# Performance work log

Hardware: AMD Instinct MI355X
Metric: run time of the kernel (lower is better)

## Reference

```python
import jax, jax.numpy as jnp
import numpy as np

B, ENC_T, DEC_T = 16, 512, 800
D = 256    # pos_att_dim == att_dim == encoder dim
H = 1024   # attention rnn dim
M = 8      # num gmm mixtures
DELTA_MIN_LIMIT = 0.0
DELTA_OFFSET = 0.0


def setup_inputs() -> dict:
    key = jax.random.key(0)
    ks = jax.random.split(key, 12)
    s = 0.05  # small init so sigmoids/tanh stay in sane range
    b_lin = jnp.concatenate([jnp.zeros((M,)), jnp.zeros((M,)), 3.0 * jnp.ones((M,))])
    return {
        'encoder_outputs': jax.random.normal(ks[0], (B, ENC_T, D), jnp.float32),
        'melenc_outputs': jax.random.normal(ks[1], (B, DEC_T, D), jnp.float32),
        'encoder_lengths': jax.random.randint(ks[2], (B,), ENC_T // 2, ENC_T + 1),
        'output_lengths': jax.random.randint(ks[3], (B,), DEC_T // 2, DEC_T + 1),
        'cond_lens': jax.random.randint(ks[4], (B,), ENC_T // 2, ENC_T + 1),
        'W_ih': jax.random.normal(ks[5], (4 * H, 3 * D), jnp.float32) * s,
        'W_hh': jax.random.normal(ks[6], (4 * H, H), jnp.float32) * s,
        'b_ih': jnp.zeros((4 * H,), jnp.float32),
        'b_hh': jnp.zeros((4 * H,), jnp.float32),
        'W1': jax.random.normal(ks[7], (D, H), jnp.float32) * s,
        'b1': jnp.zeros((D,), jnp.float32),
        'W2': jax.random.normal(ks[8], (D, D), jnp.float32) * s,
        'W_lin': jax.random.normal(ks[9], (3 * M, D), jnp.float32) * 0.01,  # lin.weight.data.mul_(0.01)
        'b_lin': b_lin,
    }


def reference(encoder_outputs, melenc_outputs, encoder_lengths, output_lengths,
              cond_lens, W_ih, W_hh, b_ih, b_hh, W1, b1, W2, W_lin, b_lin):
    Bb, enc_T, Dd = encoder_outputs.shape
    dec_T = melenc_outputs.shape[1]
    n_mix = W_lin.shape[0] // 3
    Hh = W_hh.shape[1]
    dtype = encoder_outputs.dtype

    pos = jnp.arange(enc_T, dtype=dtype)                      # [enc_T]
    cond_f = cond_lens.astype(dtype)
    enc_mask = (pos[None, :] < cond_f[:, None]).astype(dtype)  # [B, enc_T]
    cond_min1 = cond_f - 1.0                                   # [B]
    # dec-step validity mask (get_mask_3d decoder axis), [dec_T, B]
    dec_valid = (jnp.arange(dec_T)[:, None] < output_lengths[None, :]).astype(dtype)

    def lstm_cell(x, h, c):
        g = x @ W_ih.T + b_ih + h @ W_hh.T + b_hh   # [B, 4H]
        i, f, gg, o = jnp.split(g, 4, axis=-1)
        c2 = jax.nn.sigmoid(f) * c + jax.nn.sigmoid(i) * jnp.tanh(gg)
        h2 = jax.nn.sigmoid(o) * jnp.tanh(c2)
        return h2, c2

    def step(carry, xs):
        h, c, ctx, nctx, loc = carry
        mel, vdec = xs                              # mel [B,D], vdec [B]
        q = jnp.concatenate([mel, ctx, nctx], axis=-1)  # [B, 3D]
        h, c = lstm_cell(q, h, c)
        # F network: Linear -> LeakyReLU(0.1) -> Linear(no bias) -> Tanh -> lin
        x = h @ W1.T + b1
        x = jnp.where(x >= 0, x, 0.1 * x)
        x = jnp.tanh(x @ W2.T)
        out = x @ W_lin.T + b_lin                   # [B, 3M]
        w_, d_, s_ = jnp.split(out, 3, axis=-1)
        w = jax.nn.softmax(w_, axis=-1)             # [B, M]
        std = jax.nn.sigmoid(s_)
        delta = jax.nn.sigmoid(d_) + 0.005
        if DELTA_MIN_LIMIT > 0.0:
            delta = jnp.maximum(delta, DELTA_MIN_LIMIT)
        if DELTA_OFFSET > 0.0:
            delta = delta + DELTA_OFFSET
        loc = loc + delta                           # [B, M]
        # tanh-CDF difference over positions: [B, enc_T, M]
        diff = loc[:, None, :] - pos[None, :, None]
        upper = jnp.tanh((diff + 0.5) / std[:, None, :])   # uses pos - 0.5
        lower = jnp.tanh((diff - 0.5) / std[:, None, :])   # uses pos + 0.5
        z = (upper - lower) * 0.5
        align = jnp.einsum('bem,bm->be', z, w)      # [B, enc_T]
        align = align * enc_mask * vdec[:, None]    # masked_fill_(mask, 0.0)
        next_w = jnp.roll(align, 1, axis=-1)
        ctx = jnp.einsum('be,bed->bd', align, encoder_outputs)
        nctx = jnp.einsum('be,bed->bd', next_w, encoder_outputs)
        # loc = loc - (loc - (cond_lens-1)).clamp(min=0)
        loc = loc - jnp.maximum(loc - cond_min1[:, None], 0.0)
        return (h, c, ctx, nctx, loc), (ctx, align)

    init = (jnp.zeros((Bb, Hh), dtype), jnp.zeros((Bb, Hh), dtype),
            jnp.zeros((Bb, Dd), dtype), encoder_outputs[:, 0, :],
            jnp.full((Bb, n_mix), -0.1, dtype))
    xs = (jnp.swapaxes(melenc_outputs, 0, 1), dec_valid)
    _, (ctxs, aligns) = jax.lax.scan(step, init, xs)
    attention_context = jnp.swapaxes(ctxs, 0, 1)    # [B, dec_T, D]
    attention_weights = jnp.swapaxes(aligns, 0, 1)  # [B, dec_T, enc_T]
    # final mask on attention_context over decoder steps
    attention_context = attention_context * jnp.swapaxes(dec_valid, 0, 1)[:, :, None]
    return attention_context, attention_weights
```

## Files before the change

kernel.cpp:

```cpp
#include <hip/hip_runtime.h>
#include <stdint.h>

#define DEV static __device__ __forceinline__

namespace {
constexpr int Bx = 16, ENCx = 512, DECx = 800, Dx = 256, Hx = 1024;
constexpr int NBLK = 256, NTHR = 512;
constexpr int NCHAIN = 32;

constexpr int WS_H    = 0;
constexpr int WS_X1M  = WS_H + 2*Bx*Hx;
constexpr int WS_CTX  = WS_X1M + 2*Bx*Dx;
constexpr int WS_FEND = WS_CTX + 2*2*Bx*Dx;
constexpr int IW_HC  = 0;
constexpr int IW_XC  = IW_HC + 801*16;
constexpr int IW_CC  = IW_XC + 800*16;
constexpr int IW_END = IW_CC + 800*16;
constexpr size_t CTXOUT = (size_t)Bx*DECx*Dx;

constexpr int LH_STR = 1028;
constexpr int CT_STR = 260;
constexpr int LW_H   = 0;
constexpr int LW_WHH = LW_H + 16*LH_STR;
constexpr int LDS_DYN_F = LW_WHH + 16384;
constexpr size_t SMEM_BYTES = (size_t)LDS_DYN_F * 4;
}

DEV float frcp(float x){ return __builtin_amdgcn_rcpf(x); }
DEV float sigm(float x){ return frcp(1.0f + __expf(-x)); }
DEV float ftanh(float x){
  x = fminf(fmaxf(x, -15.0f), 15.0f);
  float e = __expf(2.0f*x);
  return (e - 1.0f) * frcp(e + 1.0f);
}
DEV float wred16(float v){
  v += __shfl_xor(v, 1); v += __shfl_xor(v, 2);
  v += __shfl_xor(v, 4); v += __shfl_xor(v, 8);
  return v;
}
DEV int   ld_rlx(const int* p){ return __hip_atomic_load(p, __ATOMIC_RELAXED, __HIP_MEMORY_SCOPE_AGENT); }
DEV float ldf_c(const float* p){ return __hip_atomic_load(p, __ATOMIC_RELAXED, __HIP_MEMORY_SCOPE_AGENT); }
DEV void  stf_c(float* p, float v){ __hip_atomic_store(p, v, __ATOMIC_RELAXED, __HIP_MEMORY_SCOPE_AGENT); }
DEV void  add_cnt(int* p){ __hip_atomic_fetch_add(p, 1, __ATOMIC_RELAXED, __HIP_MEMORY_SCOPE_AGENT); }
DEV void cbar(){ asm volatile("" ::: "memory"); }

DEV void spin_fma(){
  float x = 1.0f;
  #pragma unroll
  for (int i = 0; i < 16; ++i) x = fmaf(x, 1.0000001f, 1e-9f);
  asm volatile("" :: "v"(x));
}

DEV void ld8_wait(float4 (&r)[8], const float* p){
  const float *a1=p+2048,*a2=p+4096,*a3=p+6144,*a4=p+8192,*a5=p+10240,*a6=p+12288,*a7=p+14336;
  asm volatile(
    "global_load_dwordx4 %0, %8, off sc1\n\t"
    "global_load_dwordx4 %1, %9, off sc1\n\t"
    "global_load_dwordx4 %2, %10, off sc1\n\t"
    "global_load_dwordx4 %3, %11, off sc1\n\t"
    "global_load_dwordx4 %4, %12, off sc1\n\t"
    "global_load_dwordx4 %5, %13, off sc1\n\t"
    "global_load_dwordx4 %6, %14, off sc1\n\t"
    "global_load_dwordx4 %7, %15, off sc1\n\t"
    "s_waitcnt vmcnt(0)"
    : "=&v"(r[0]),"=&v"(r[1]),"=&v"(r[2]),"=&v"(r[3]),
      "=&v"(r[4]),"=&v"(r[5]),"=&v"(r[6]),"=&v"(r[7])
    : "v"(p),"v"(a1),"v"(a2),"v"(a3),"v"(a4),"v"(a5),"v"(a6),"v"(a7)
    : "memory");
}
DEV void ld4_wait(float4 (&r)[4], const float* p){
  const float *a1=p+2048,*a2=p+4096,*a3=p+6144;
  asm volatile(
    "global_load_dwordx4 %0, %4, off sc1\n\t"
    "global_load_dwordx4 %1, %5, off sc1\n\t"
    "global_load_dwordx4 %2, %6, off sc1\n\t"
    "global_load_dwordx4 %3, %7, off sc1\n\t"
    "s_waitcnt vmcnt(0)"
    : "=&v"(r[0]),"=&v"(r[1]),"=&v"(r[2]),"=&v"(r[3])
    : "v"(p),"v"(a1),"v"(a2),"v"(a3)
    : "memory");
}

DEV void wait_cnt(int* p, int target, volatile int* lslot, int stamp){
  const int tid = threadIdx.x;
  if (tid < 64){
    while (ld_rlx(p) < target) spin_fma();
    if (tid == 0) *lslot = stamp;
  } else {
    while (*lslot < stamp) spin_fma();
  }
  __syncthreads();
  cbar();
}

DEV void gchunk(float (&acc)[2][4], float4 wa, float4 wb, const float* xlane, size_t xstride, int b4){
  #pragma unroll
  for (int bi = 0; bi < 4; ++bi){
    float4 xv = *reinterpret_cast<const float4*>(xlane + (size_t)(b4*4 + bi)*xstride);
    acc[0][bi] = fmaf(wa.x,xv.x, fmaf(wa.y,xv.y, fmaf(wa.z,xv.z, fmaf(wa.w,xv.w, acc[0][bi]))));
    acc[1][bi] = fmaf(wb.x,xv.x, fmaf(wb.y,xv.y, fmaf(wb.z,xv.z, fmaf(wb.w,xv.w, acc[1][bi]))));
  }
}

extern "C" __global__ void gmm_init(float* wsf){
  int* wsi = (int*)(wsf + WS_FEND);
  int idx = blockIdx.x*blockDim.x + threadIdx.x;
  for (int k = idx; k < IW_END; k += gridDim.x*blockDim.x) wsi[k] = 0;
}

extern "C" __global__ void __launch_bounds__(NTHR, 1) gmm_main(
    const float* __restrict__ enc, const float* __restrict__ mel,
    const int* __restrict__ outlen, const int* __restrict__ condlen,
    const float* __restrict__ Wih, const float* __restrict__ Whh,
    const float* __restrict__ bih, const float* __restrict__ bhh,
    const float* __restrict__ W1,  const float* __restrict__ b1v,
    const float* __restrict__ W2,  const float* __restrict__ Wlin,
    const float* __restrict__ blin,
    float* __restrict__ out, float* __restrict__ wsf)
{
  const int bk = blockIdx.x, tid = threadIdx.x;
  const int lane = tid & 63;
  const int klane4 = (tid & 15) * 4;
  const int b4 = (tid >> 4) & 3;
  const int wid = tid >> 6;

  int* wsi  = (int*)(wsf + WS_FEND);
  int* hCnt = wsi + IW_HC;
  int* xCnt = wsi + IW_XC;
  int* cCnt = wsi + IW_CC;
  float* hm   = wsf + WS_H;
  float* x1m  = wsf + WS_X1M;
  float* ctxm = wsf + WS_CTX;

  extern __shared__ float lds[];
  float* lh   = lds + LW_H;
  float* lwhh = lds + LW_WHH;

  __shared__ float g_lds[256];
  __shared__ float bsum[16];
  __shared__ float cl[64];
  __shared__ float x1l[256];
  __shared__ float x2p[512];
  __shared__ float x2l[256];
  __shared__ float outp[384];
  __shared__ float outl[24];
  __shared__ float mixw[8], mixlc[8], mixis[8];
  __shared__ float locl[8];
  __shared__ float albl[512];
  __shared__ float cpn[2][4][128];
  __shared__ int   s_cond, s_olen;
  __shared__ int   lfh, lfx, lfc;

  if (tid == 0){ lfh = 0; lfx = 0; lfc = 0; }

  const int jidx0 = 2*wid;
  const int j0 = (jidx0 >> 2)*1024 + bk*4 + (jidx0 & 3);
  const int j1 = ((jidx0+1) >> 2)*1024 + bk*4 + ((jidx0+1) & 3);
  const float* WihR0 = Wih + (size_t)j0*768;
  const float* WihR1 = Wih + (size_t)j1*768;

  const bool is_chain = (bk < NCHAIN);
  const int  cb  = bk >> 1;
  const int  hf2 = bk & 1;

  #pragma unroll
  for (int jj = jidx0; jj <= jidx0 + 1; ++jj){
    const int gj = (jj >> 2)*1024 + bk*4 + (jj & 3);
    float4* dst = (float4*)(lwhh + jj*1024);
    const float4* s = (const float4*)(Whh + (size_t)gj*1024);
    for (int i = lane; i < 256; i += 64) dst[i] = s[i];
  }
  if (tid < 16){
    int g = tid >> 2, ul = tid & 3, u = bk*4 + ul;
    bsum[tid] = bih[g*1024 + u] + bhh[g*1024 + u];
  }
  float4 w2r[32];
  if (is_chain){
    if (tid == 0){ s_cond = condlen[cb]; s_olen = outlen[cb]; }
    if (tid < 8) locl[tid] = -0.1f;
    int r = tid >> 1, hf = tid & 1;
    const float* w2row = W2 + (size_t)r*256 + hf*128;
    #pragma unroll
    for (int i = 0; i < 32; ++i) w2r[i] = *reinterpret_cast<const float4*>(w2row + i*4);
  }
  __syncthreads();

  auto write_h = [&](int t){
    float4 r[8];
    ld8_wait(r, hm + (t & 1)*(Bx*Hx) + tid*4);
    #pragma unroll
    for (int i = 0; i < 8; ++i){
      int rr = 2*i + (tid >> 8);
      *reinterpret_cast<float4*>(lh + rr*LH_STR + (tid & 255)*4) = r[i];
    }
    __syncthreads();
  };

  {
    float acc[2][4] = {{0,0,0,0},{0,0,0,0}};
    #pragma unroll
    for (int it = 0; it < 4; ++it){
      int k = it*64 + klane4;
      gchunk(acc, *(const float4*)(WihR0 + k), *(const float4*)(WihR1 + k),
             mel + k, (size_t)DECx*Dx, b4);
    }
    #pragma unroll
    for (int it = 0; it < 4; ++it){
      int k = it*64 + klane4;
      gchunk(acc, *(const float4*)(WihR0 + 512 + k), *(const float4*)(WihR1 + 512 + k),
             enc + k, (size_t)ENCx*Dx, b4);
    }
    #pragma unroll
    for (int jj = 0; jj < 2; ++jj)
      #pragma unroll
      for (int bi = 0; bi < 4; ++bi){
        float v = wred16(acc[jj][bi]);
        if ((tid & 15) == 0) g_lds[(jidx0 + jj)*16 + b4*4 + bi] = v;
      }
    __syncthreads();
    if (tid < 64){
      int b = tid & 15, ul = tid >> 4, u = bk*4 + ul;
      float gi = g_lds[( 0 + ul)*16 + b] + bsum[ul];
      float gg = g_lds[( 8 + ul)*16 + b] + bsum[8 + ul];
      float go = g_lds[(12 + ul)*16 + b] + bsum[12 + ul];
      float c2 = sigm(gi) * ftanh(gg);
      float h2 = sigm(go) * ftanh(c2);
      cl[b*4 + ul] = c2;
      stf_c(hm + b*1024 + u, h2);
    }
    __syncthreads();
    if (tid == 0) add_cnt(hCnt + 0*16);
  }

  for (int t = 0; t < DECx; ++t){
    const int par = t & 1;
    const bool last = (t == DECx - 1);

    wait_cnt(hCnt + t*16, NBLK, &lfh, t + 1);
    write_h(t);
    if (tid < 256){
      int b = tid >> 4, kl = tid & 15;
      const float* W1r = W1 + (size_t)bk*1024;
      float a = 0.f;
      #pragma unroll
      for (int it = 0; it < 16; ++it){
        int k = it*64 + kl*4;
        float4 wv = *reinterpret_cast<const float4*>(W1r + k);
        float4 xv = *reinterpret_cast<const float4*>(lh + (size_t)b*LH_STR + k);
        a = fmaf(wv.x,xv.x, fmaf(wv.y,xv.y, fmaf(wv.z,xv.z, fmaf(wv.w,xv.w, a))));
      }
      a = wred16(a);
      if (kl == 0){
        a += b1v[bk];
        a = (a >= 0.f) ? a : 0.1f*a;
        stf_c(x1m + par*(Bx*Dx) + b*256 + bk, a);
      }
    }
    __syncthreads();
    if (tid == 0) add_cnt(xCnt + t*16);

    float acc[2][4] = {{0,0,0,0},{0,0,0,0}};

    if (is_chain){
      wait_cnt(xCnt + t*16, NBLK, &lfx, t + 1);
      if (tid < 256) x1l[tid] = ldf_c(x1m + par*(Bx*Dx) + cb*256 + tid);
      __syncthreads();
      {
        int hf = tid & 1;
        const float* x1b = x1l + hf*128;
        float a = 0.f;
        #pragma unroll
        for (int i = 0; i < 32; ++i){
          float4 xv = *(const float4*)(x1b + i*4);
          a = fmaf(w2r[i].x,xv.x, fmaf(w2r[i].y,xv.y, fmaf(w2r[i].z,xv.z, fmaf(w2r[i].w,xv.w, a))));
        }
        x2p[tid] = a;
      }
      __syncthreads();
      if (tid < 256) x2l[tid] = ftanh(x2p[2*tid] + x2p[2*tid + 1]);
      __syncthreads();
      if (tid < 384){
        int r = tid >> 4, ks = tid & 15;
        const float* wr = Wlin + (size_t)r*256 + ks*16;
        const float* xb = x2l + ks*16;
        float s = 0.f;
        #pragma unroll
        for (int k = 0; k < 16; ++k) s = fmaf(xb[k], wr[k], s);
        outp[tid] = s;
      }
      __syncthreads();
      if (tid < 24){
        float s = blin[tid];
        #pragma unroll
        for (int j = 0; j < 16; ++j) s += outp[tid*16 + j];
        outl[tid] = s;
      }
      __syncthreads();
      if (tid < 8){
        float w = outl[tid];
        float mx = w;
        mx = fmaxf(mx, __shfl_xor(mx, 1)); mx = fmaxf(mx, __shfl_xor(mx, 2)); mx = fmaxf(mx, __shfl_xor(mx, 4));
        float e = __expf(w - mx);
        float sum = e;
        sum += __shfl_xor(sum, 1); sum += __shfl_xor(sum, 2); sum += __shfl_xor(sum, 4);
        mixw[tid] = e * frcp(sum);
        float cm1 = (float)s_cond - 1.0f;
        float dl = sigm(outl[8 + tid]) + 0.005f;
        float lc = locl[tid] + dl;
        mixlc[tid] = lc;
        locl[tid]  = fminf(lc, cm1);
        mixis[tid] = 1.0f + __expf(-outl[16 + tid]);
      }
      __syncthreads();
      {
        int e = tid;
        float ef = (float)e;
        float a = 0.f;
        #pragma unroll
        for (int m = 0; m < 8; ++m){
          float df = mixlc[m] - ef;
          a += (ftanh((df + 0.5f)*mixis[m]) - ftanh((df - 0.5f)*mixis[m])) * mixw[m];
        }
        a *= 0.5f;
        bool valid = (e < s_cond) && (t < s_olen);
        if (!valid) a = 0.f;
        albl[e] = a;
        if (hf2 == 0)
          out[CTXOUT + (size_t)cb*((size_t)DECx*ENCx) + (size_t)t*ENCx + e] = a;
      }
      __syncthreads();
      {
        int dl = tid & 127, eg = tid >> 7;
        const float* encb = enc + (size_t)cb*ENCx*Dx + hf2*128;
        float ca = 0.f, na = 0.f;
        #pragma unroll 4
        for (int i = 0; i < 128; ++i){
          int e = eg*128 + i;
          float av = albl[e];
          float nv = albl[(e + 511) & 511];
          float ev = encb[(size_t)e*256 + dl];
          ca = fmaf(av, ev, ca);
          na = fmaf(nv, ev, na);
        }
        cpn[0][eg][dl & 127] = 0.f;
        cpn[0][eg][dl] = ca;
        cpn[1][eg][dl] = na;
      }
      __syncthreads();
      if (tid < 256){
        int z = tid >> 7, dd = tid & 127;
        float s = cpn[z][0][dd] + cpn[z][1][dd] + cpn[z][2][dd] + cpn[z][3][dd];
        int d = hf2*128 + dd;
        stf_c(ctxm + par*(2*Bx*Dx) + z*(Bx*Dx) + cb*256 + d, s);
        if (z == 0)
          out[(size_t)cb*((size_t)DECx*Dx) + (size_t)t*Dx + d] = s;
      }
      __syncthreads();
      if (tid == 0) add_cnt(cCnt + t*16);
      if (!last){
        const float* melt = mel + (size_t)(t + 1)*Dx;
        #pragma unroll
        for (int it = 0; it < 4; ++it){
          int k = it*64 + klane4;
          gchunk(acc, *(const float4*)(WihR0 + k), *(const float4*)(WihR1 + k),
                 melt + k, (size_t)DECx*Dx, b4);
        }
        #pragma unroll 4
        for (int it = 0; it < 16; ++it){
          int k = it*64 + klane4;
          gchunk(acc, *(const float4*)(lwhh + jidx0*1024 + k), *(const float4*)(lwhh + (jidx0+1)*1024 + k),
                 lh + k, LH_STR, b4);
        }
      }
    } else {
      if (!last){
        const float* melt = mel + (size_t)(t + 1)*Dx;
        #pragma unroll
        for (int it = 0; it < 4; ++it){
          int k = it*64 + klane4;
          gchunk(acc, *(const float4*)(WihR0 + k), *(const float4*)(WihR1 + k),
                 melt + k, (size_t)DECx*Dx, b4);
        }
        #pragma unroll 4
        for (int it = 0; it < 16; ++it){
          int k = it*64 + klane4;
          gchunk(acc, *(const float4*)(lwhh + jidx0*1024 + k), *(const float4*)(lwhh + (jidx0+1)*1024 + k),
                 lh + k, LH_STR, b4);
        }
      }
    }

    if (!last){
      wait_cnt(cCnt + t*16, NCHAIN, &lfc, t + 1);
      {
        float4 cr[4];
        ld4_wait(cr, ctxm + par*(2*Bx*Dx) + tid*4);
        #pragma unroll
        for (int i = 0; i < 4; ++i){
          int r = 8*i + (tid >> 6);
          *reinterpret_cast<float4*>(lh + r*CT_STR + (tid & 63)*4) = cr[i];
        }
      }
      __syncthreads();
      #pragma unroll
      for (int it = 0; it < 4; ++it){
        int k = it*64 + klane4;
        gchunk(acc, *(const float4*)(WihR0 + 256 + k), *(const float4*)(WihR1 + 256 + k),
               lh + k, CT_STR, b4);
      }
      #pragma unroll
      for (int it = 0; it < 4; ++it){
        int k = it*64 + klane4;
        gchunk(acc, *(const float4*)(WihR0 + 512 + k), *(const float4*)(WihR1 + 512 + k),
               lh + 16*CT_STR + k, CT_STR, b4);
      }
      #pragma unroll
      for (int jj = 0; jj < 2; ++jj)
        #pragma unroll
        for (int bi = 0; bi < 4; ++bi){
          float v = wred16(acc[jj][bi]);
          if ((tid & 15) == 0) g_lds[(jidx0 + jj)*16 + b4*4 + bi] = v;
        }
      __syncthreads();
      if (tid < 64){
        int b = tid & 15, ul = tid >> 4, u = bk*4 + ul;
        float gi = g_lds[( 0 + ul)*16 + b] + bsum[ul];
        float gf = g_lds[( 4 + ul)*16 + b] + bsum[4 + ul];
        float gg = g_lds[( 8 + ul)*16 + b] + bsum[8 + ul];
        float go = g_lds[(12 + ul)*16 + b] + bsum[12 + ul];
        float co = cl[b*4 + ul];
        float c2 = sigm(gf)*co + sigm(gi)*ftanh(gg);
        float h2 = sigm(go)*ftanh(c2);
        cl[b*4 + ul] = c2;
        stf_c(hm + ((t + 1) & 1)*(Bx*Hx) + b*1024 + u, h2);
      }
      __syncthreads();
      if (tid == 0) add_cnt(hCnt + (t + 1)*16);
    }
  }
}

extern "C" void kernel_launch(void* const* d_in, const int* in_sizes, int n_in,
                              void* d_out, int out_size, void* d_ws, size_t ws_size,
                              hipStream_t stream)
{
  const float* enc    = (const float*)d_in[0];
  const float* mel    = (const float*)d_in[1];
  const int*   outlen = (const int*)d_in[3];
  const int*   cond   = (const int*)d_in[4];
  const float* Wih    = (const float*)d_in[5];
  const float* Whh    = (const float*)d_in[6];
  const float* bih    = (const float*)d_in[7];
  const float* bhh    = (const float*)d_in[8];
  const float* W1     = (const float*)d_in[9];
  const float* b1v    = (const float*)d_in[10];
  const float* W2     = (const float*)d_in[11];
  const float* Wlin   = (const float*)d_in[12];
  const float* blin   = (const float*)d_in[13];
  float* outp = (float*)d_out;
  float* wsf  = (float*)d_ws;

  (void)hipFuncSetAttribute((const void*)gmm_main,
                            hipFuncAttributeMaxDynamicSharedMemorySize,
                            (int)SMEM_BYTES);

  hipLaunchKernelGGL(gmm_init, dim3(64), dim3(256), 0, stream, wsf);

  void* args[] = {
    (void*)&enc, (void*)&mel, (void*)&outlen, (void*)&cond,
    (void*)&Wih, (void*)&Whh, (void*)&bih, (void*)&bhh,
    (void*)&W1, (void*)&b1v, (void*)&W2, (void*)&Wlin, (void*)&blin,
    (void*)&outp, (void*)&wsf
  };
  (void)hipLaunchCooperativeKernel((void*)gmm_main, dim3(NBLK), dim3(NTHR),
                                   args, SMEM_BYTES, stream);
}
```

Measured before the change: 60.04 ms.

## Split persistent kernel into gate and chain blocks with bf16 exchange and slot flags

```diff
diff --git a/kernel.cpp b/kernel.cpp
--- a/kernel.cpp
+++ b/kernel.cpp
@@ -5,17 +5,19 @@
 
 namespace {
 constexpr int Bx = 16, ENCx = 512, DECx = 800, Dx = 256, Hx = 1024;
-constexpr int NBLK = 256, NTHR = 512;
-constexpr int NCHAIN = 32;
-
-constexpr int WS_H    = 0;
-constexpr int WS_X1M  = WS_H + 2*Bx*Hx;
-constexpr int WS_CTX  = WS_X1M + 2*Bx*Dx;
-constexpr int WS_FEND = WS_CTX + 2*2*Bx*Dx;
-constexpr int IW_HC  = 0;
-constexpr int IW_XC  = IW_HC + 801*16;
-constexpr int IW_CC  = IW_XC + 800*16;
-constexpr int IW_END = IW_CC + 800*16;
+constexpr int NGATE = 128, NCHAIN = 32, NBLK = NGATE + NCHAIN, NTHR = 512;
+
+constexpr int WS_HBH  = 0;
+constexpr int WS_CTXH = WS_HBH + 16384;
+constexpr int WS_X1M  = WS_CTXH + 8192;
+constexpr int WS_FEND = WS_X1M + 8192;
+constexpr int IW_HSLOT = 0;
+constexpr int IW_XSLOT = 128;
+constexpr int IW_CSLOT = 256;
+constexpr int IW_HRDY  = 320;
+constexpr int IW_XRDY  = 448;
+constexpr int IW_CRDY  = 576;
+constexpr int IW_END   = 704;
 constexpr size_t CTXOUT = (size_t)Bx*DECx*Dx;
 
 constexpr int LH_STR = 1028;
@@ -39,35 +41,22 @@
   return v;
 }
 DEV int   ld_rlx(const int* p){ return __hip_atomic_load(p, __ATOMIC_RELAXED, __HIP_MEMORY_SCOPE_AGENT); }
+DEV void  st_rlx(int* p, int v){ __hip_atomic_store(p, v, __ATOMIC_RELAXED, __HIP_MEMORY_SCOPE_AGENT); }
+DEV void  st_rlx_u32(unsigned* p, unsigned v){ __hip_atomic_store(p, v, __ATOMIC_RELAXED, __HIP_MEMORY_SCOPE_AGENT); }
 DEV float ldf_c(const float* p){ return __hip_atomic_load(p, __ATOMIC_RELAXED, __HIP_MEMORY_SCOPE_AGENT); }
 DEV void  stf_c(float* p, float v){ __hip_atomic_store(p, v, __ATOMIC_RELAXED, __HIP_MEMORY_SCOPE_AGENT); }
-DEV void  add_cnt(int* p){ __hip_atomic_fetch_add(p, 1, __ATOMIC_RELAXED, __HIP_MEMORY_SCOPE_AGENT); }
 DEV void cbar(){ asm volatile("" ::: "memory"); }
 
-DEV void spin_fma(){
-  float x = 1.0f;
-  #pragma unroll
-  for (int i = 0; i < 16; ++i) x = fmaf(x, 1.0000001f, 1e-9f);
-  asm volatile("" :: "v"(x));
-}
-
-DEV void ld8_wait(float4 (&r)[8], const float* p){
-  const float *a1=p+2048,*a2=p+4096,*a3=p+6144,*a4=p+8192,*a5=p+10240,*a6=p+12288,*a7=p+14336;
-  asm volatile(
-    "global_load_dwordx4 %0, %8, off sc1\n\t"
-    "global_load_dwordx4 %1, %9, off sc1\n\t"
-    "global_load_dwordx4 %2, %10, off sc1\n\t"
-    "global_load_dwordx4 %3, %11, off sc1\n\t"
-    "global_load_dwordx4 %4, %12, off sc1\n\t"
-    "global_load_dwordx4 %5, %13, off sc1\n\t"
-    "global_load_dwordx4 %6, %14, off sc1\n\t"
-    "global_load_dwordx4 %7, %15, off sc1\n\t"
-    "s_waitcnt vmcnt(0)"
-    : "=&v"(r[0]),"=&v"(r[1]),"=&v"(r[2]),"=&v"(r[3]),
-      "=&v"(r[4]),"=&v"(r[5]),"=&v"(r[6]),"=&v"(r[7])
-    : "v"(p),"v"(a1),"v"(a2),"v"(a3),"v"(a4),"v"(a5),"v"(a6),"v"(a7)
-    : "memory");
-}
+DEV unsigned pack_bf16(float lo, float hi){
+  unsigned a = __builtin_bit_cast(unsigned, lo);
+  unsigned b = __builtin_bit_cast(unsigned, hi);
+  a += 0x7FFFu + ((a >> 16) & 1u);
+  b += 0x7FFFu + ((b >> 16) & 1u);
+  return (a >> 16) | (b & 0xFFFF0000u);
+}
+DEV float bflo(unsigned w){ return __builtin_bit_cast(float, w << 16); }
+DEV float bfhi(unsigned w){ return __builtin_bit_cast(float, w & 0xFFFF0000u); }
+
 DEV void ld4_wait(float4 (&r)[4], const float* p){
   const float *a1=p+2048,*a2=p+4096,*a3=p+6144;
   asm volatile(
@@ -80,26 +69,56 @@
     : "v"(p),"v"(a1),"v"(a2),"v"(a3)
     : "memory");
 }
-
-DEV void wait_cnt(int* p, int target, volatile int* lslot, int stamp){
+DEV void ld2_wait(float4 (&r)[2], const float* p){
+  const float *a1=p+2048;
+  asm volatile(
+    "global_load_dwordx4 %0, %2, off sc1\n\t"
+    "global_load_dwordx4 %1, %3, off sc1\n\t"
+    "s_waitcnt vmcnt(0)"
+    : "=&v"(r[0]),"=&v"(r[1])
+    : "v"(p),"v"(a1)
+    : "memory");
+}
+DEV int4 ld4i_sc1(const int* p){
+  int4 r;
+  asm volatile("global_load_dwordx4 %0, %1, off sc1\n\ts_waitcnt vmcnt(0)"
+    : "=&v"(r) : "v"(p) : "memory");
+  return r;
+}
+
+DEV void wait_rdy(int* rdy8, int repl, int target, volatile int* lslot){
   const int tid = threadIdx.x;
   if (tid < 64){
-    while (ld_rlx(p) < target) spin_fma();
-    if (tid == 0) *lslot = stamp;
+    while (ld_rlx(rdy8 + repl*16) < target) __builtin_amdgcn_s_sleep(8);
+    if (tid == 0) *lslot = target;
   } else {
-    while (*lslot < stamp) spin_fma();
+    while (*lslot < target) __builtin_amdgcn_s_sleep(1);
   }
   __syncthreads();
   cbar();
 }
 
-DEV void gchunk(float (&acc)[2][4], float4 wa, float4 wb, const float* xlane, size_t xstride, int b4){
-  #pragma unroll
-  for (int bi = 0; bi < 4; ++bi){
-    float4 xv = *reinterpret_cast<const float4*>(xlane + (size_t)(b4*4 + bi)*xstride);
-    acc[0][bi] = fmaf(wa.x,xv.x, fmaf(wa.y,xv.y, fmaf(wa.z,xv.z, fmaf(wa.w,xv.w, acc[0][bi]))));
-    acc[1][bi] = fmaf(wb.x,xv.x, fmaf(wb.y,xv.y, fmaf(wb.z,xv.z, fmaf(wb.w,xv.w, acc[1][bi]))));
+DEV void detect_pub(int* slots, int nq, int* rdy8, int target, volatile int* lslot){
+  const int tid = threadIdx.x;
+  if (tid < 64){
+    const int* my = slots + tid*4;
+    const bool active = (tid < nq);
+    for (;;){
+      bool ok = true;
+      if (active){
+        int4 v = ld4i_sc1(my);
+        ok = (v.x >= target) & (v.y >= target) & (v.z >= target) & (v.w >= target);
+      }
+      if (__ballot(ok) == ~0ull) break;
+      __builtin_amdgcn_s_sleep(8);
+    }
+    if (tid < 8) st_rlx(rdy8 + tid*16, target);
+    if (tid == 0) *lslot = target;
+  } else {
+    while (*lslot < target) __builtin_amdgcn_s_sleep(1);
   }
+  __syncthreads();
+  cbar();
 }
 
 extern "C" __global__ void gmm_init(float* wsf){
@@ -119,26 +138,30 @@
     float* __restrict__ out, float* __restrict__ wsf)
 {
   const int bk = blockIdx.x, tid = threadIdx.x;
-  const int lane = tid & 63;
   const int klane4 = (tid & 15) * 4;
   const int b4 = (tid >> 4) & 3;
   const int wid = tid >> 6;
 
-  int* wsi  = (int*)(wsf + WS_FEND);
-  int* hCnt = wsi + IW_HC;
-  int* xCnt = wsi + IW_XC;
-  int* cCnt = wsi + IW_CC;
-  float* hm   = wsf + WS_H;
-  float* x1m  = wsf + WS_X1M;
-  float* ctxm = wsf + WS_CTX;
+  int* wsi   = (int*)(wsf + WS_FEND);
+  int* hslot = wsi + IW_HSLOT;
+  int* xslot = wsi + IW_XSLOT;
+  int* cslot = wsi + IW_CSLOT;
+  int* hrdy  = wsi + IW_HRDY;
+  int* xrdy  = wsi + IW_XRDY;
+  int* crdy  = wsi + IW_CRDY;
+  unsigned short* hbh = (unsigned short*)(wsf + WS_HBH);
+  unsigned* ctx32u    = (unsigned*)(wsf + WS_CTXH);
+  float* x1m = wsf + WS_X1M;
 
   extern __shared__ float lds[];
-  float* lh   = lds + LW_H;
-  float* lwhh = lds + LW_WHH;
-
-  __shared__ float g_lds[256];
-  __shared__ float bsum[16];
-  __shared__ float cl[64];
+  float*    lh      = lds + LW_H;
+  unsigned* lwhh_u  = (unsigned*)(lds + LW_WHH);
+  const uint2* lwhh2 = (const uint2*)(lds + LW_WHH);
+
+  __shared__ float g_lds[512];
+  __shared__ float bsum[32];
+  __shared__ float cl[128];
+  __shared__ float hstg[128];
   __shared__ float x1l[256];
   __shared__ float x2p[512];
   __shared__ float x2l[256];
@@ -153,29 +176,34 @@
 
   if (tid == 0){ lfh = 0; lfx = 0; lfc = 0; }
 
-  const int jidx0 = 2*wid;
-  const int j0 = (jidx0 >> 2)*1024 + bk*4 + (jidx0 & 3);
-  const int j1 = ((jidx0+1) >> 2)*1024 + bk*4 + ((jidx0+1) & 3);
-  const float* WihR0 = Wih + (size_t)j0*768;
-  const float* WihR1 = Wih + (size_t)j1*768;
-
-  const bool is_chain = (bk < NCHAIN);
-  const int  cb  = bk >> 1;
-  const int  hf2 = bk & 1;
-
-  #pragma unroll
-  for (int jj = jidx0; jj <= jidx0 + 1; ++jj){
-    const int gj = (jj >> 2)*1024 + bk*4 + (jj & 3);
-    float4* dst = (float4*)(lwhh + jj*1024);
-    const float4* s = (const float4*)(Whh + (size_t)gj*1024);
-    for (int i = lane; i < 256; i += 64) dst[i] = s[i];
+  const bool is_gate = (bk < NGATE);
+  const int  cid = bk - NGATE;
+  const int  cb  = cid >> 1;
+  const int  hf2 = cid & 1;
+  const int  repl = bk & 7;
+
+  const int r0 = wid*4;
+  const float* wih[4];
+  if (is_gate){
+    #pragma unroll
+    for (int r = 0; r < 4; ++r){
+      int lr = r0 + r;
+      wih[r] = Wih + (size_t)((lr>>3)*1024 + bk*8 + (lr&7))*768;
+    }
   }
-  if (tid < 16){
-    int g = tid >> 2, ul = tid & 3, u = bk*4 + ul;
-    bsum[tid] = bih[g*1024 + u] + bhh[g*1024 + u];
-  }
+
   float4 w2r[32];
-  if (is_chain){
+  if (is_gate){
+    for (int i = tid; i < 16384; i += NTHR){
+      int r = i >> 9, c = i & 511;
+      size_t gr = (size_t)((r>>3)*1024 + bk*8 + (r&7));
+      lwhh_u[i] = pack_bf16(Whh[gr*1024 + 2*c], Whh[gr*1024 + 2*c + 1]);
+    }
+    if (tid < 32){
+      int g = tid >> 3, u = bk*8 + (tid & 7);
+      bsum[tid] = bih[g*1024 + u] + bhh[g*1024 + u];
+    }
+  } else {
     if (tid == 0){ s_cond = condlen[cb]; s_olen = outlen[cb]; }
     if (tid < 8) locl[tid] = -0.1f;
     int r = tid >> 1, hf = tid & 1;
@@ -186,84 +214,211 @@
   __syncthreads();
 
   auto write_h = [&](int t){
-    float4 r[8];
-    ld8_wait(r, hm + (t & 1)*(Bx*Hx) + tid*4);
+    float4 r[4];
+    ld4_wait(r, (const float*)(hbh + (t & 1)*16384) + tid*4);
     #pragma unroll
-    for (int i = 0; i < 8; ++i){
-      int rr = 2*i + (tid >> 8);
-      *reinterpret_cast<float4*>(lh + rr*LH_STR + (tid & 255)*4) = r[i];
+    for (int i = 0; i < 4; ++i){
+      unsigned wx = __builtin_bit_cast(unsigned, r[i].x);
+      unsigned wy = __builtin_bit_cast(unsigned, r[i].y);
+      unsigned wz = __builtin_bit_cast(unsigned, r[i].z);
+      unsigned ww = __builtin_bit_cast(unsigned, r[i].w);
+      int b = i*4 + (tid >> 7);
+      float* d = lh + b*LH_STR + (tid & 127)*8;
+      d[0] = bflo(wx); d[1] = bfhi(wx); d[2] = bflo(wy); d[3] = bfhi(wy);
+      d[4] = bflo(wz); d[5] = bfhi(wz); d[6] = bflo(ww); d[7] = bfhi(ww);
     }
     __syncthreads();
   };
 
-  {
-    float acc[2][4] = {{0,0,0,0},{0,0,0,0}};
+  auto cell_and_publish = [&](float (&acc)[4][4], int bsel, int stamp, bool first){
+    #pragma unroll
+    for (int r = 0; r < 4; ++r)
+      #pragma unroll
+      for (int bi = 0; bi < 4; ++bi){
+        float v = wred16(acc[r][bi]);
+        if ((tid & 15) == 0) g_lds[(r0 + r)*16 + b4*4 + bi] = v;
+      }
+    __syncthreads();
+    if (tid < 128){
+      int u = tid >> 4, b = tid & 15;
+      float gi = g_lds[( 0 + u)*16 + b] + bsum[u];
+      float gg = g_lds[(16 + u)*16 + b] + bsum[16 + u];
+      float go = g_lds[(24 + u)*16 + b] + bsum[24 + u];
+      float c2;
+      if (first){
+        c2 = sigm(gi) * ftanh(gg);
+      } else {
+        float gf = g_lds[(8 + u)*16 + b] + bsum[8 + u];
+        c2 = sigm(gf)*cl[tid] + sigm(gi)*ftanh(gg);
+      }
+      float h2 = sigm(go)*ftanh(c2);
+      cl[tid] = c2;
+      hstg[u*16 + b] = h2;
+    }
+    __syncthreads();
+    if (tid < 64){
+      int p = tid >> 4, b = tid & 15;
+      unsigned w = pack_bf16(hstg[(2*p)*16 + b], hstg[(2*p + 1)*16 + b]);
+      st_rlx_u32((unsigned*)hbh + bsel*8192 + b*512 + bk*4 + p, w);
+    }
+    __syncthreads();
+    if (tid == 0) st_rlx(hslot + bk, stamp);
+  };
+
+  if (is_gate){
+    float acc[4][4] = {};
     #pragma unroll
     for (int it = 0; it < 4; ++it){
       int k = it*64 + klane4;
-      gchunk(acc, *(const float4*)(WihR0 + k), *(const float4*)(WihR1 + k),
-             mel + k, (size_t)DECx*Dx, b4);
+      float4 wv[4];
+      #pragma unroll
+      for (int r = 0; r < 4; ++r) wv[r] = *reinterpret_cast<const float4*>(wih[r] + k);
+      #pragma unroll
+      for (int bi = 0; bi < 4; ++bi){
+        float4 xv = *reinterpret_cast<const float4*>(mel + (size_t)(b4*4 + bi)*DECx*Dx + k);
+        #pragma unroll
+        for (int r = 0; r < 4; ++r)
+          acc[r][bi] = fmaf(wv[r].x,xv.x, fmaf(wv[r].y,xv.y, fmaf(wv[r].z,xv.z, fmaf(wv[r].w,xv.w, acc[r][bi]))));
+      }
     }
     #pragma unroll
     for (int it = 0; it < 4; ++it){
       int k = it*64 + klane4;
-      gchunk(acc, *(const float4*)(WihR0 + 512 + k), *(const float4*)(WihR1 + 512 + k),
-             enc + k, (size_t)ENCx*Dx, b4);
-    }
-    #pragma unroll
-    for (int jj = 0; jj < 2; ++jj)
+      float4 wv[4];
+      #pragma unroll
+      for (int r = 0; r < 4; ++r) wv[r] = *reinterpret_cast<const float4*>(wih[r] + 512 + k);
       #pragma unroll
       for (int bi = 0; bi < 4; ++bi){
-        float v = wred16(acc[jj][bi]);
-        if ((tid & 15) == 0) g_lds[(jidx0 + jj)*16 + b4*4 + bi] = v;
-      }
-    __syncthreads();
-    if (tid < 64){
-      int b = tid & 15, ul = tid >> 4, u = bk*4 + ul;
-      float gi = g_lds[( 0 + ul)*16 + b] + bsum[ul];
-      float gg = g_lds[( 8 + ul)*16 + b] + bsum[8 + ul];
-      float go = g_lds[(12 + ul)*16 + b] + bsum[12 + ul];
-      float c2 = sigm(gi) * ftanh(gg);
-      float h2 = sigm(go) * ftanh(c2);
-      cl[b*4 + ul] = c2;
-      stf_c(hm + b*1024 + u, h2);
-    }
-    __syncthreads();
-    if (tid == 0) add_cnt(hCnt + 0*16);
+        float4 xv = *reinterpret_cast<const float4*>(enc + (size_t)(b4*4 + bi)*ENCx*Dx + k);
+        #pragma unroll
+        for (int r = 0; r < 4; ++r)
+          acc[r][bi] = fmaf(wv[r].x,xv.x, fmaf(wv[r].y,xv.y, fmaf(wv[r].z,xv.z, fmaf(wv[r].w,xv.w, acc[r][bi]))));
+      }
+    }
+    cell_and_publish(acc, 0, 1, true);
   }
 
   for (int t = 0; t < DECx; ++t){
     const int par = t & 1;
     const bool last = (t == DECx - 1);
 
-    wait_cnt(hCnt + t*16, NBLK, &lfh, t + 1);
-    write_h(t);
-    if (tid < 256){
-      int b = tid >> 4, kl = tid & 15;
-      const float* W1r = W1 + (size_t)bk*1024;
-      float a = 0.f;
-      #pragma unroll
-      for (int it = 0; it < 16; ++it){
-        int k = it*64 + kl*4;
-        float4 wv = *reinterpret_cast<const float4*>(W1r + k);
-        float4 xv = *reinterpret_cast<const float4*>(lh + (size_t)b*LH_STR + k);
-        a = fmaf(wv.x,xv.x, fmaf(wv.y,xv.y, fmaf(wv.z,xv.z, fmaf(wv.w,xv.w, a))));
-      }
-      a = wred16(a);
-      if (kl == 0){
-        a += b1v[bk];
-        a = (a >= 0.f) ? a : 0.1f*a;
-        stf_c(x1m + par*(Bx*Dx) + b*256 + bk, a);
-      }
-    }
-    __syncthreads();
-    if (tid == 0) add_cnt(xCnt + t*16);
-
-    float acc[2][4] = {{0,0,0,0},{0,0,0,0}};
-
-    if (is_chain){
-      wait_cnt(xCnt + t*16, NBLK, &lfx, t + 1);
-      if (tid < 256) x1l[tid] = ldf_c(x1m + par*(Bx*Dx) + cb*256 + tid);
+    if (is_gate){
+      if (bk == 0) detect_pub(hslot, 32, hrdy, t + 1, &lfh);
+      else         wait_rdy(hrdy, repl, t + 1, &lfh);
+      write_h(t);
+
+      {
+        int row = tid >> 8;
+        int b = (tid >> 4) & 15, kl = tid & 15;
+        const float* W1r = W1 + (size_t)(2*bk + row)*1024;
+        float a = 0.f;
+        #pragma unroll
+        for (int it = 0; it < 16; ++it){
+          int k = it*64 + kl*4;
+          float4 wv = *reinterpret_cast<const float4*>(W1r + k);
+          float4 xv = *reinterpret_cast<const float4*>(lh + (size_t)b*LH_STR + k);
+          a = fmaf(wv.x,xv.x, fmaf(wv.y,xv.y, fmaf(wv.z,xv.z, fmaf(wv.w,xv.w, a))));
+        }
+        a = wred16(a);
+        if (kl == 0){
+          a += b1v[2*bk + row];
+          a = (a >= 0.f) ? a : 0.1f*a;
+          stf_c(x1m + par*4096 + b*256 + 2*bk + row, a);
+        }
+      }
+      __syncthreads();
+      if (tid == 0) st_rlx(xslot + bk, t + 1);
+
+      float acc[4][4] = {};
+      if (!last){
+        const int tt = t + 1;
+        #pragma unroll
+        for (int it = 0; it < 4; ++it){
+          int k = it*64 + klane4;
+          float4 wv[4];
+          #pragma unroll
+          for (int r = 0; r < 4; ++r) wv[r] = *reinterpret_cast<const float4*>(wih[r] + k);
+          #pragma unroll
+          for (int bi = 0; bi < 4; ++bi){
+            float4 xv = *reinterpret_cast<const float4*>(mel + ((size_t)(b4*4 + bi)*DECx + tt)*Dx + k);
+            #pragma unroll
+            for (int r = 0; r < 4; ++r)
+              acc[r][bi] = fmaf(wv[r].x,xv.x, fmaf(wv[r].y,xv.y, fmaf(wv[r].z,xv.z, fmaf(wv[r].w,xv.w, acc[r][bi]))));
+          }
+        }
+        #pragma unroll 4
+        for (int it = 0; it < 16; ++it){
+          int k = it*64 + klane4;
+          uint2 wv2[4];
+          #pragma unroll
+          for (int r = 0; r < 4; ++r) wv2[r] = lwhh2[(size_t)(r0 + r)*256 + it*16 + (tid & 15)];
+          #pragma unroll
+          for (int bi = 0; bi < 4; ++bi){
+            float4 xv = *reinterpret_cast<const float4*>(lh + (size_t)(b4*4 + bi)*LH_STR + k);
+            #pragma unroll
+            for (int r = 0; r < 4; ++r){
+              float w0 = bflo(wv2[r].x), w1 = bfhi(wv2[r].x);
+              float w2 = bflo(wv2[r].y), w3 = bfhi(wv2[r].y);
+              acc[r][bi] = fmaf(w0,xv.x, fmaf(w1,xv.y, fmaf(w2,xv.z, fmaf(w3,xv.w, acc[r][bi]))));
+            }
+          }
+        }
+      }
+
+      if (!last){
+        if (bk == 0) detect_pub(cslot, 8, crdy, t + 1, &lfc);
+        else         wait_rdy(crdy, repl, t + 1, &lfc);
+        {
+          float4 cr[2];
+          ld2_wait(cr, (const float*)(ctx32u + par*4096) + tid*4);
+          #pragma unroll
+          for (int i = 0; i < 2; ++i){
+            unsigned wx = __builtin_bit_cast(unsigned, cr[i].x);
+            unsigned wy = __builtin_bit_cast(unsigned, cr[i].y);
+            unsigned wz = __builtin_bit_cast(unsigned, cr[i].z);
+            unsigned ww = __builtin_bit_cast(unsigned, cr[i].w);
+            int base = i*2048 + tid*4;
+            int z = base >> 11, b = (base >> 7) & 15, j = base & 127;
+            float* d = lh + (z*16 + b)*CT_STR + 2*j;
+            d[0] = bflo(wx); d[1] = bfhi(wx); d[2] = bflo(wy); d[3] = bfhi(wy);
+            d[4] = bflo(wz); d[5] = bfhi(wz); d[6] = bflo(ww); d[7] = bfhi(ww);
+          }
+        }
+        __syncthreads();
+        #pragma unroll
+        for (int it = 0; it < 4; ++it){
+          int k = it*64 + klane4;
+          float4 wv[4];
+          #pragma unroll
+          for (int r = 0; r < 4; ++r) wv[r] = *reinterpret_cast<const float4*>(wih[r] + 256 + k);
+          #pragma unroll
+          for (int bi = 0; bi < 4; ++bi){
+            float4 xv = *reinterpret_cast<const float4*>(lh + (size_t)(b4*4 + bi)*CT_STR + k);
+            #pragma unroll
+            for (int r = 0; r < 4; ++r)
+              acc[r][bi] = fmaf(wv[r].x,xv.x, fmaf(wv[r].y,xv.y, fmaf(wv[r].z,xv.z, fmaf(wv[r].w,xv.w, acc[r][bi]))));
+          }
+        }
+        #pragma unroll
+        for (int it = 0; it < 4; ++it){
+          int k = it*64 + klane4;
+          float4 wv[4];
+          #pragma unroll
+          for (int r = 0; r < 4; ++r) wv[r] = *reinterpret_cast<const float4*>(wih[r] + 512 + k);
+          #pragma unroll
+          for (int bi = 0; bi < 4; ++bi){
+            float4 xv = *reinterpret_cast<const float4*>(lh + (size_t)(16 + b4*4 + bi)*CT_STR + k);
+            #pragma unroll
+            for (int r = 0; r < 4; ++r)
+              acc[r][bi] = fmaf(wv[r].x,xv.x, fmaf(wv[r].y,xv.y, fmaf(wv[r].z,xv.z, fmaf(wv[r].w,xv.w, acc[r][bi]))));
+          }
+        }
+        cell_and_publish(acc, (t + 1) & 1, t + 2, false);
+      }
+    } else {
+      if (bk == NGATE) detect_pub(xslot, 32, xrdy, t + 1, &lfx);
+      else             wait_rdy(xrdy, repl, t + 1, &lfx);
+      if (tid < 256) x1l[tid] = ldf_c(x1m + par*4096 + cb*256 + tid);
       __syncthreads();
       {
         int hf = tid & 1;
@@ -313,8 +468,7 @@
       }
       __syncthreads();
       {
-        int e = tid;
-        float ef = (float)e;
+        float ef = (float)tid;
         float a = 0.f;
         #pragma unroll
         for (int m = 0; m < 8; ++m){
@@ -322,11 +476,11 @@
           a += (ftanh((df + 0.5f)*mixis[m]) - ftanh((df - 0.5f)*mixis[m])) * mixw[m];
         }
         a *= 0.5f;
-        bool valid = (e < s_cond) && (t < s_olen);
+        bool valid = (tid < s_cond) && (t < s_olen);
         if (!valid) a = 0.f;
-        albl[e] = a;
+        albl[tid] = a;
         if (hf2 == 0)
-          out[CTXOUT + (size_t)cb*((size_t)DECx*ENCx) + (size_t)t*ENCx + e] = a;
+          out[CTXOUT + (size_t)cb*((size_t)DECx*ENCx) + (size_t)t*ENCx + tid] = a;
       }
       __syncthreads();
       {
@@ -342,7 +496,6 @@
           ca = fmaf(av, ev, ca);
           na = fmaf(nv, ev, na);
         }
-        cpn[0][eg][dl & 127] = 0.f;
         cpn[0][eg][dl] = ca;
         cpn[1][eg][dl] = na;
       }
@@ -350,92 +503,18 @@
       if (tid < 256){
         int z = tid >> 7, dd = tid & 127;
         float s = cpn[z][0][dd] + cpn[z][1][dd] + cpn[z][2][dd] + cpn[z][3][dd];
-        int d = hf2*128 + dd;
-        stf_c(ctxm + par*(2*Bx*Dx) + z*(Bx*Dx) + cb*256 + d, s);
+        x2p[z*128 + dd] = s;
         if (z == 0)
-          out[(size_t)cb*((size_t)DECx*Dx) + (size_t)t*Dx + d] = s;
-      }
-      __syncthreads();
-      if (tid == 0) add_cnt(cCnt + t*16);
-      if (!last){
-        const float* melt = mel + (size_t)(t + 1)*Dx;
-        #pragma unroll
-        for (int it = 0; it < 4; ++it){
-          int k = it*64 + klane4;
-          gchunk(acc, *(const float4*)(WihR0 + k), *(const float4*)(WihR1 + k),
-                 melt + k, (size_t)DECx*Dx, b4);
-        }
-        #pragma unroll 4
-        for (int it = 0; it < 16; ++it){
-          int k = it*64 + klane4;
-          gchunk(acc, *(const float4*)(lwhh + jidx0*1024 + k), *(const float4*)(lwhh + (jidx0+1)*1024 + k),
-                 lh + k, LH_STR, b4);
-        }
-      }
-    } else {
-      if (!last){
-        const float* melt = mel + (size_t)(t + 1)*Dx;
-        #pragma unroll
-        for (int it = 0; it < 4; ++it){
-          int k = it*64 + klane4;
-          gchunk(acc, *(const float4*)(WihR0 + k), *(const float4*)(WihR1 + k),
-                 melt + k, (size_t)DECx*Dx, b4);
-        }
-        #pragma unroll 4
-        for (int it = 0; it < 16; ++it){
-          int k = it*64 + klane4;
-          gchunk(acc, *(const float4*)(lwhh + jidx0*1024 + k), *(const float4*)(lwhh + (jidx0+1)*1024 + k),
-                 lh + k, LH_STR, b4);
-        }
-      }
-    }
-
-    if (!last){
-      wait_cnt(cCnt + t*16, NCHAIN, &lfc, t + 1);
-      {
-        float4 cr[4];
-        ld4_wait(cr, ctxm + par*(2*Bx*Dx) + tid*4);
-        #pragma unroll
-        for (int i = 0; i < 4; ++i){
-          int r = 8*i + (tid >> 6);
-          *reinterpret_cast<float4*>(lh + r*CT_STR + (tid & 63)*4) = cr[i];
-        }
-      }
-      __syncthreads();
-      #pragma unroll
-      for (int it = 0; it < 4; ++it){
-        int k = it*64 + klane4;
-        gchunk(acc, *(const float4*)(WihR0 + 256 + k), *(const float4*)(WihR1 + 256 + k),
-               lh + k, CT_STR, b4);
-      }
-      #pragma unroll
-      for (int it = 0; it < 4; ++it){
-        int k = it*64 + klane4;
-        gchunk(acc, *(const float4*)(WihR0 + 512 + k), *(const float4*)(WihR1 + 512 + k),
-               lh + 16*CT_STR + k, CT_STR, b4);
-      }
-      #pragma unroll
-      for (int jj = 0; jj < 2; ++jj)
-        #pragma unroll
-        for (int bi = 0; bi < 4; ++bi){
-          float v = wred16(acc[jj][bi]);
-          if ((tid & 15) == 0) g_lds[(jidx0 + jj)*16 + b4*4 + bi] = v;
-        }
-      __syncthreads();
-      if (tid < 64){
-        int b = tid & 15, ul = tid >> 4, u = bk*4 + ul;
-        float gi = g_lds[( 0 + ul)*16 + b] + bsum[ul];
-        float gf = g_lds[( 4 + ul)*16 + b] + bsum[4 + ul];
-        float gg = g_lds[( 8 + ul)*16 + b] + bsum[8 + ul];
-        float go = g_lds[(12 + ul)*16 + b] + bsum[12 + ul];
-        float co = cl[b*4 + ul];
-        float c2 = sigm(gf)*co + sigm(gi)*ftanh(gg);
-        float h2 = sigm(go)*ftanh(c2);
-        cl[b*4 + ul] = c2;
-        stf_c(hm + ((t + 1) & 1)*(Bx*Hx) + b*1024 + u, h2);
-      }
-      __syncthreads();
-      if (tid == 0) add_cnt(hCnt + (t + 1)*16);
+          out[(size_t)cb*((size_t)DECx*Dx) + (size_t)t*Dx + hf2*128 + dd] = s;
+      }
+      __syncthreads();
+      if (tid < 128){
+        int z = tid >> 6, j = tid & 63;
+        unsigned w = pack_bf16(x2p[z*128 + 2*j], x2p[z*128 + 2*j + 1]);
+        st_rlx_u32(ctx32u + par*4096 + z*2048 + cb*128 + hf2*64 + j, w);
+      }
+      __syncthreads();
+      if (tid == 0) st_rlx(cslot + cid, t + 1);
     }
   }
 }
@@ -464,7 +543,7 @@
                             hipFuncAttributeMaxDynamicSharedMemorySize,
                             (int)SMEM_BYTES);
 
-  hipLaunchKernelGGL(gmm_init, dim3(64), dim3(256), 0, stream, wsf);
+  hipLaunchKernelGGL(gmm_init, dim3(16), dim3(64), 0, stream, wsf);
 
   void* args[] = {
     (void*)&enc, (void*)&mel, (void*)&outlen, (void*)&cond,
```

After: 50.26 ms. 1.19x faster.
